# Performance work log

Measured on AMD Instinct MI355X. Metric: run time of the kernel, lower is better.

The kernel has to match this reference:

```python
import jax, jax.numpy as jnp
import numpy as np

B, T, C, H = 2, 2048, 1024, 16
D = C // H  # head_dim = 64


def setup_inputs() -> dict:
    key = jax.random.key(0)
    ks = jax.random.split(key, 5)
    s = 1.0 / np.sqrt(C)
    return {
        "x": jax.random.normal(ks[0], (B, T, C), jnp.float32),
        "Wq": jax.random.normal(ks[1], (C, C), jnp.float32) * s,
        "bq": jnp.zeros((C,), jnp.float32),
        "Wk": jax.random.normal(ks[2], (C, C), jnp.float32) * s,
        "bk": jnp.zeros((C,), jnp.float32),
        "Wv": jax.random.normal(ks[3], (C, C), jnp.float32) * s,
        "bv": jnp.zeros((C,), jnp.float32),
        "Wo": jax.random.normal(ks[4], (C, C), jnp.float32) * s,
        "bo": jnp.zeros((C,), jnp.float32),
    }


def reference(x, Wq, bq, Wk, bk, Wv, bv, Wo, bo):
    Bx, Tx, Cx = x.shape
    # torch Linear: y = x @ W.T + b
    q = (x @ Wq.T + bq).reshape(Bx, Tx, H, D).transpose(0, 2, 1, 3)  # [B,H,T,D]
    k = (x @ Wk.T + bk).reshape(Bx, Tx, H, D).transpose(0, 2, 1, 3)
    v = (x @ Wv.T + bv).reshape(Bx, Tx, H, D).transpose(0, 2, 1, 3)
    att = jnp.einsum("bhqd,bhkd->bhqk", q, k) / np.sqrt(D).astype(np.float32)
    mask = jnp.tril(jnp.ones((Tx, Tx), bool))  # causal mask [T,T]
    att = jnp.where(mask, att, -jnp.inf)
    att = jax.nn.softmax(att, axis=-1)
    out = jnp.einsum("bhqk,bhkd->bhqd", att, v)
    out = out.transpose(0, 2, 1, 3).reshape(Bx, Tx, Cx)
    return out @ Wo.T + bo
```

## Files before the change

### kernel.cpp

```cpp
#include <hip/hip_runtime.h>
#include <hip/hip_bf16.h>

#define B_ 2
#define T_ 2048
#define C_ 1024
#define H_ 16
#define D_ 64

typedef unsigned short u16;
typedef __bf16 bf16x8 __attribute__((ext_vector_type(8)));
typedef float floatx4 __attribute__((ext_vector_type(4)));

__device__ __forceinline__ float bf2f(u16 u) {
  union { unsigned int i; float f; } x; x.i = ((unsigned int)u) << 16; return x.f;
}
__device__ __forceinline__ u16 f2bf(float f) {
  union { float f; unsigned int i; } x; x.f = f;
  unsigned int r = x.i + 0x7fffu + ((x.i >> 16) & 1u);
  return (u16)(r >> 16);
}

__device__ __forceinline__ unsigned cvtpk(float lo, float hi) {
  unsigned r;
  asm("v_cvt_pk_bf16_f32 %0, %1, %2" : "=v"(r) : "v"(lo), "v"(hi));
  return r;
}

__device__ __forceinline__ void gld16(void* lds, const void* g) {
  __builtin_amdgcn_global_load_lds(
      (const __attribute__((address_space(1))) unsigned int*)g,
      (__attribute__((address_space(3))) unsigned int*)lds, 16, 0, 0);
}

#define NXF4 1048576
#define NWF4 262144

__global__ __launch_bounds__(256) void cvt_all(
    const float* __restrict__ x,  const float* __restrict__ Wq,
    const float* __restrict__ Wk, const float* __restrict__ Wv,
    const float* __restrict__ Wo, u16* __restrict__ dst_base)
{
  const int i = blockIdx.x * 256 + threadIdx.x;
  const float* src; size_t off;
  if (i < NXF4)               { src = x;  off = i; }
  else if (i < NXF4 + NWF4)   { src = Wq; off = i - NXF4; }
  else if (i < NXF4 + 2*NWF4) { src = Wk; off = i - (NXF4 + NWF4); }
  else if (i < NXF4 + 3*NWF4) { src = Wv; off = i - (NXF4 + 2*NWF4); }
  else                        { src = Wo; off = i - (NXF4 + 3*NWF4); }
  float4 f = ((const float4*)src)[off];
  ushort4 o;
  o.x = f2bf(f.x); o.y = f2bf(f.y); o.z = f2bf(f.z); o.w = f2bf(f.w);
  ((ushort4*)dst_base)[i] = o;
}

#define QSCALE 0.1803368801111f

#define PBAR()                                                \
  do {                                                        \
    asm volatile("" ::: "memory");                            \
    __builtin_amdgcn_s_barrier();                             \
    asm volatile("s_waitcnt lgkmcnt(0)" ::: "memory");        \
  } while (0)

#define EBAR()                                                \
  do {                                                        \
    asm volatile("" ::: "memory");                            \
    __builtin_amdgcn_s_barrier();                             \
    asm volatile("" ::: "memory");                            \
  } while (0)

__global__ __launch_bounds__(512, 2) void gemm_qkv8(
    const u16* __restrict__ X, const u16* __restrict__ Wb,
    const float* __restrict__ b0, const float* __restrict__ b1,
    const float* __restrict__ b2,
    u16* __restrict__ Yq, u16* __restrict__ Yk, u16* __restrict__ Yv)
{
  __shared__ __align__(16) u16 L[57344];

  const int tid  = threadIdx.x;
  const int lane = tid & 63;
  const int m16  = lane & 15;
  const int q4   = lane >> 4;
  const int wv   = tid >> 6;
  const int wm   = wv >> 2;
  const int wn   = wv & 3;

  const int bid = blockIdx.x;
  const int xcd = bid & 7;
  const int idx = bid >> 3;
  const int bx  = (xcd & 3) * 4 + (idx & 3);
  const int by  = (xcd >> 2) * 8 + (idx >> 2);

  const u16* Abase  = X  + (size_t)bx * 256 * C_;
  const u16* Bbase  = Wb + (size_t)by * 192 * C_;
  const u16* A1base = Abase + (size_t)128 * C_;

  const int rB  = tid >> 3;
  const int s0 = tid,       r0 = rB;
  const int s1 = tid + 512, r1 = 64 + rB;
  const int k0a = ((tid & 7) ^ (rB & 7)) * 8;

#define STAGE_A(dsthalf, srcrows, kofs)                                       \
  do {                                                                        \
    gld16(&(dsthalf)[s0 * 8], (srcrows) + (size_t)r0 * C_ + (kofs) + k0a);    \
    gld16(&(dsthalf)[s1 * 8], (srcrows) + (size_t)r1 * C_ + (kofs) + k0a);    \
  } while (0)

#define STAGE_BL(dstB, srcrows, kofs, l)                                      \
  gld16(&(dstB)[((l) * 512 + tid) * 8],                                       \
        (srcrows) + (size_t)((l) * 64 + rB) * C_ + (kofs) + k0a)

  u16* buf0 = L;
  u16* buf1 = L + 28672;

  STAGE_BL(buf0 + 16384, Bbase, 0, 0);
  STAGE_BL(buf0 + 16384, Bbase, 0, 1);
  STAGE_BL(buf0 + 16384, Bbase, 0, 2);
  STAGE_A (buf0,         Abase,  0);
  STAGE_A (buf0 + 8192,  A1base, 0);
  STAGE_BL(buf1 + 16384, Bbase, 64, 0);
  STAGE_BL(buf1 + 16384, Bbase, 64, 1);
  STAGE_A (buf1,         Abase, 64);
  asm volatile("s_waitcnt vmcnt(4)" ::: "memory");
  __builtin_amdgcn_s_barrier();
  asm volatile("" ::: "memory");

  floatx4 acc[8][3] = {};

  const int a0off = m16 * 64 + ((q4      ^ (lane & 7)) * 8);
  const int a1off = m16 * 64 + (((q4 + 4) ^ (lane & 7)) * 8);
  const int bro   = wn * 3072;

  for (int i = 0; i < 16; ++i) {
    u16* buf  = (i & 1) ? buf1 : buf0;
    u16* bufn = (i & 1) ? buf0 : buf1;
    const u16* Ah = buf + wm * 8192;
    const u16* Bh = buf + 16384;
    const bool p1 = (i + 1) < 16;
    const bool p2 = (i + 2) < 16;
    const int  k1 = (i + 1) * 64;
    const int  k2 = (i + 2) * 64;

    bf16x8 a[4][2], bA[2][2], bB[2];

#pragma unroll
    for (int f = 0; f < 4; ++f) {
      a[f][0] = *(const bf16x8*)&Ah[f * 1024 + a0off];
      a[f][1] = *(const bf16x8*)&Ah[f * 1024 + a1off];
    }
#pragma unroll
    for (int g = 0; g < 2; ++g) {
      bA[g][0] = *(const bf16x8*)&Bh[bro + g * 1024 + a0off];
      bA[g][1] = *(const bf16x8*)&Bh[bro + g * 1024 + a1off];
    }
    if (p1) STAGE_A(bufn + 8192, A1base, k1);
    PBAR();
    __builtin_amdgcn_s_setprio(1);
#pragma unroll
    for (int f = 0; f < 4; ++f)
#pragma unroll
      for (int g = 0; g < 2; ++g) {
        acc[f][g] = __builtin_amdgcn_mfma_f32_16x16x32_bf16(a[f][0], bA[g][0], acc[f][g], 0, 0, 0);
        acc[f][g] = __builtin_amdgcn_mfma_f32_16x16x32_bf16(a[f][1], bA[g][1], acc[f][g], 0, 0, 0);
      }
    __builtin_amdgcn_s_setprio(0);
    EBAR();

    bB[0] = *(const bf16x8*)&Bh[bro + 2048 + a0off];
    bB[1] = *(const bf16x8*)&Bh[bro + 2048 + a1off];
    if (p1) STAGE_BL(bufn + 16384, Bbase, k1, 2);
    PBAR();
    __builtin_amdgcn_s_setprio(1);
#pragma unroll
    for (int f = 0; f < 4; ++f) {
      acc[f][2] = __builtin_amdgcn_mfma_f32_16x16x32_bf16(a[f][0], bB[0], acc[f][2], 0, 0, 0);
      acc[f][2] = __builtin_amdgcn_mfma_f32_16x16x32_bf16(a[f][1], bB[1], acc[f][2], 0, 0, 0);
    }
    __builtin_amdgcn_s_setprio(0);
    EBAR();

#pragma unroll
    for (int f = 0; f < 4; ++f) {
      a[f][0] = *(const bf16x8*)&Ah[4096 + f * 1024 + a0off];
      a[f][1] = *(const bf16x8*)&Ah[4096 + f * 1024 + a1off];
    }
    if (p2) {
      STAGE_BL(buf + 16384, Bbase, k2, 0);
      STAGE_BL(buf + 16384, Bbase, k2, 1);
    }
    PBAR();
    __builtin_amdgcn_s_setprio(1);
#pragma unroll
    for (int f = 0; f < 4; ++f) {
      acc[4 + f][2] = __builtin_amdgcn_mfma_f32_16x16x32_bf16(a[f][0], bB[0], acc[4 + f][2], 0, 0, 0);
      acc[4 + f][2] = __builtin_amdgcn_mfma_f32_16x16x32_bf16(a[f][1], bB[1], acc[4 + f][2], 0, 0, 0);
    }
    __builtin_amdgcn_s_setprio(0);
    EBAR();

    if (p2) STAGE_A(buf, Abase, k2);
    PBAR();
    __builtin_amdgcn_s_setprio(1);
#pragma unroll
    for (int f = 0; f < 4; ++f)
#pragma unroll
      for (int g = 0; g < 2; ++g) {
        acc[4 + f][g] = __builtin_amdgcn_mfma_f32_16x16x32_bf16(a[f][0], bA[g][0], acc[4 + f][g], 0, 0, 0);
        acc[4 + f][g] = __builtin_amdgcn_mfma_f32_16x16x32_bf16(a[f][1], bA[g][1], acc[4 + f][g], 0, 0, 0);
      }
    __builtin_amdgcn_s_setprio(0);
    asm volatile("" ::: "memory");
    if (p2) asm volatile("s_waitcnt vmcnt(4)" ::: "memory");
    else    asm volatile("s_waitcnt vmcnt(0)" ::: "memory");
    __builtin_amdgcn_s_barrier();
    asm volatile("" ::: "memory");
  }

  const int mbase = bx * 256 + wm * 128 + q4 * 4;
#pragma unroll
  for (int nf = 0; nf < 3; ++nf) {
    const int nzg = by * 192 + wn * 48 + nf * 16 + m16;
    const int z  = nzg >> 10;
    const int nl = nzg & 1023;
    const int h = nl >> 6, d = nl & (D_ - 1);
    const float bv = (z == 0 ? b0 : z == 1 ? b1 : b2)[nl];
    if (z == 2) {
#pragma unroll
      for (int mf = 0; mf < 8; ++mf) {
        const int m  = mbase + mf * 16;
        const int bb = m >> 11, t = m & (T_ - 1);
        ushort4 pk;
        pk.x = f2bf(acc[mf][nf][0] + bv);
        pk.y = f2bf(acc[mf][nf][1] + bv);
        pk.z = f2bf(acc[mf][nf][2] + bv);
        pk.w = f2bf(acc[mf][nf][3] + bv);
        *(ushort4*)&Yv[(((size_t)bb * H_ + h) * D_ + d) * T_ + t] = pk;
      }
    } else {
      u16* Y = z ? Yk : Yq;
      const float sc = z ? 1.0f : QSCALE;
#pragma unroll
      for (int mf = 0; mf < 8; ++mf) {
        const int m  = mbase + mf * 16;
        const int bb = m >> 11, tq = m & (T_ - 1);
#pragma unroll
        for (int r = 0; r < 4; ++r) {
          Y[(((size_t)bb * H_ + h) * T_ + (tq + r)) * D_ + d] =
              f2bf((acc[mf][nf][r] + bv) * sc);
        }
      }
    }
  }
}

__global__ __launch_bounds__(256) void gemm_out(
    const u16* __restrict__ X, const u16* __restrict__ W,
    const float* __restrict__ bias, float* __restrict__ Yf)
{
  const int K = C_, N = C_;
  __shared__ __align__(16) u16 As[128 * 32];
  __shared__ __align__(16) u16 Bs[128 * 32];

  const int tid  = threadIdx.x;
  const int wv   = tid >> 6;
  const int lane = tid & 63;
  const int mcol = lane & 15;
  const int quad = lane >> 4;
  const int wr = wv >> 1, wc = wv & 1;
  const int m0 = blockIdx.x * 128;
  const int n0 = blockIdx.y * 128;

  const int srow = tid >> 2;
  const int scol = (tid & 3) * 8;
  const u16* xp0 = X + (size_t)(m0 + srow) * K + scol;
  const u16* xp1 = xp0 + (size_t)64 * K;
  const u16* wp0 = W + (size_t)(n0 + srow) * K + scol;
  const u16* wp1 = wp0 + (size_t)64 * K;

  floatx4 acc[4][4] = {};

  for (int k0 = 0; k0 < K; k0 += 32) {
    gld16(&As[tid * 8],        xp0 + k0);
    gld16(&As[2048 + tid * 8], xp1 + k0);
    gld16(&Bs[tid * 8],        wp0 + k0);
    gld16(&Bs[2048 + tid * 8], wp1 + k0);
    __syncthreads();

    bf16x8 a[4], b[4];
#pragma unroll
    for (int rf = 0; rf < 4; ++rf)
      a[rf] = *(const bf16x8*)&As[(wr * 64 + rf * 16 + mcol) * 32 + quad * 8];
#pragma unroll
    for (int cf = 0; cf < 4; ++cf)
      b[cf] = *(const bf16x8*)&Bs[(wc * 64 + cf * 16 + mcol) * 32 + quad * 8];
#pragma unroll
    for (int rf = 0; rf < 4; ++rf)
#pragma unroll
      for (int cf = 0; cf < 4; ++cf)
        acc[rf][cf] = __builtin_amdgcn_mfma_f32_16x16x32_bf16(
            a[rf], b[cf], acc[rf][cf], 0, 0, 0);
    __syncthreads();
  }

#pragma unroll
  for (int cf = 0; cf < 4; ++cf) {
    const int n = n0 + wc * 64 + cf * 16 + mcol;
    const float bv = bias[n];
#pragma unroll
    for (int rf = 0; rf < 4; ++rf) {
#pragma unroll
      for (int r = 0; r < 4; ++r) {
        const int m = m0 + wr * 64 + rf * 16 + quad * 4 + r;
        Yf[(size_t)m * N + n] = acc[rf][cf][r] + bv;
      }
    }
  }
}

#define KSB 4096
#define VTB 4096

__constant__ unsigned char CH_T[24]  = {7,15,15,14,14,6,13,13, 4,10,10,5,11,11,12,12, 9,9,8,8,3,2,1,0};
__constant__ unsigned char CH_J0[24] = {0,0,16,0,15,0,0,14,   0,0,11,0,0,12,0,13,    0,10,0,9,0,0,0,0};
__constant__ unsigned char CH_J1[24] = {15,15,31,14,29,13,13,27, 9,10,21,11,11,23,12,25, 9,19,8,17,7,5,3,1};
__constant__ unsigned char CH_P[24]  = {0,1,2,1,2,0,1,2,      0,1,2,0,1,2,1,2,       1,2,1,2,0,0,0,0};

__global__ __launch_bounds__(256, 3) void attn_flash(
    const u16* __restrict__ Q, const u16* __restrict__ K,
    const u16* __restrict__ Vg, u16* __restrict__ O,
    float* __restrict__ OP, float* __restrict__ LP)
{
  __shared__ __align__(16) u16 Ks[2 * KSB];
  __shared__ __align__(16) u16 Vt[2 * VTB];

  const int tid  = threadIdx.x;
  const int wv   = tid >> 6;
  const int lane = tid & 63;
  const int mcol = lane & 15;
  const int quad = lane >> 4;

  const int bx = blockIdx.x;
  const int bh = bx & 31;
  const int c  = bx >> 5;
  const int t  = CH_T[c];
  const int j0 = CH_J0[c];
  const int j1 = CH_J1[c];
  const int pm = CH_P[c];
  const int ti = pm ? ((bh * 8 + (t - 8)) * 2 + (pm - 1)) : 0;

  const size_t base  = (size_t)bh * T_ * D_;
  const size_t vbase = (size_t)bh * D_ * T_;
  const int b = bh >> 4, h = bh & (H_ - 1);

  bf16x8 vones;
  {
    const u16 ov = (mcol == 0) ? (u16)0x3F80 : (u16)0;
    union { u16 s[8]; bf16x8 v; } tmp;
#pragma unroll
    for (int i = 0; i < 8; ++i) tmp.s[i] = ov;
    vones = tmp.v;
  }

  const int srow = lane >> 3;
  const int sg   = (lane & 7) ^ srow;
  const int c0 = wv * 2, c1 = wv * 2 + 1;
  const int sl0 = (quad ^ (mcol & 7)) * 8;

  const size_t koff0 = base + (size_t)(c0 * 8 + srow) * D_ + sg * 8;
  const size_t koff1 = base + (size_t)(c1 * 8 + srow) * D_ + sg * 8;
  const size_t voff0 = vbase + (size_t)(c0 * 8 + srow) * T_ + sg * 8;
  const size_t voff1 = vbase + (size_t)(c1 * 8 + srow) * T_ + sg * 8;

  const u16* qg = Q + base + (size_t)(t * 128 + wv * 32 + mcol) * D_ + quad * 8;
  const bf16x8 qf[2][2] = {
    { *(const bf16x8*)qg,             *(const bf16x8*)(qg + 32) },
    { *(const bf16x8*)(qg + 16 * D_), *(const bf16x8*)(qg + 16 * D_ + 32) }
  };

  floatx4 oacc[2][5] = {};

  {
    const size_t kj = (size_t)j0 * 64 * D_;
    const int    vj = j0 * 64;
    gld16(&Ks[c0 * 512 + lane * 8], K  + koff0 + kj);
    gld16(&Ks[c1 * 512 + lane * 8], K  + koff1 + kj);
    gld16(&Vt[c0 * 512 + lane * 8], Vg + voff0 + vj);
    gld16(&Vt[c1 * 512 + lane * 8], Vg + voff1 + vj);
  }

  for (int j = j0; j <= j1; ++j) {
    const int cur = (j - j0) & 1;
    __syncthreads();

    if (j < j1) {
      const int nb = cur ^ 1;
      const size_t kj = (size_t)(j + 1) * 64 * D_;
      const int    vj = (j + 1) * 64;
      gld16(&Ks[nb * KSB + c0 * 512 + lane * 8], K  + koff0 + kj);
      gld16(&Ks[nb * KSB + c1 * 512 + lane * 8], K  + koff1 + kj);
      gld16(&Vt[nb * VTB + c0 * 512 + lane * 8], Vg + voff0 + vj);
      gld16(&Vt[nb * VTB + c1 * 512 + lane * 8], Vg + voff1 + vj);
    }

    const u16* ksb = &Ks[cur * KSB];
    const u16* vtb = &Vt[cur * VTB];

    floatx4 sacc[2][4] = {};
    __builtin_amdgcn_s_setprio(1);
#pragma unroll
    for (int nt = 0; nt < 4; ++nt) {
      const u16* kr = &ksb[(nt * 16 + mcol) * 64];
      bf16x8 kb0 = *(const bf16x8*)&kr[sl0];
      bf16x8 kb1 = *(const bf16x8*)&kr[sl0 ^ 32];
      sacc[0][nt] = __builtin_amdgcn_mfma_f32_16x16x32_bf16(kb0, qf[0][0], sacc[0][nt], 0, 0, 0);
      sacc[0][nt] = __builtin_amdgcn_mfma_f32_16x16x32_bf16(kb1, qf[0][1], sacc[0][nt], 0, 0, 0);
      sacc[1][nt] = __builtin_amdgcn_mfma_f32_16x16x32_bf16(kb0, qf[1][0], sacc[1][nt], 0, 0, 0);
      sacc[1][nt] = __builtin_amdgcn_mfma_f32_16x16x32_bf16(kb1, qf[1][1], sacc[1][nt], 0, 0, 0);
    }
    __builtin_amdgcn_s_setprio(0);

    const int dj = j - 2 * t;
    if (dj >= 0) {
#pragma unroll
      for (int hf = 0; hf < 2; ++hf) {
        const int klim = wv * 32 + hf * 16 + mcol - dj * 64;
#pragma unroll
        for (int nt = 0; nt < 4; ++nt)
#pragma unroll
          for (int r = 0; r < 4; ++r)
            if (nt * 16 + quad * 4 + r > klim) sacc[hf][nt][r] = -1e30f;
      }
    }

    bf16x8 pa[2][2];
#pragma unroll
    for (int hf = 0; hf < 2; ++hf) {
      unsigned w[4][2];
#pragma unroll
      for (int nt = 0; nt < 4; ++nt)
#pragma unroll
        for (int i = 0; i < 2; ++i)
          w[nt][i] = cvtpk(exp2f(sacc[hf][nt][2*i]), exp2f(sacc[hf][nt][2*i+1]));
      union { unsigned u[4]; bf16x8 v; } p0, p1;
#pragma unroll
      for (int i = 0; i < 2; ++i) {
        unsigned x = w[0][i], y = w[1][i];
        asm("v_permlane32_swap_b32 %0, %1" : "+v"(x), "+v"(y));
        asm("v_permlane16_swap_b32 %0, %1" : "+v"(x), "+v"(y));
        p0.u[i] = x; p0.u[i + 2] = y;
        unsigned x2 = w[2][i], y2 = w[3][i];
        asm("v_permlane32_swap_b32 %0, %1" : "+v"(x2), "+v"(y2));
        asm("v_permlane16_swap_b32 %0, %1" : "+v"(x2), "+v"(y2));
        p1.u[i] = x2; p1.u[i + 2] = y2;
      }
      pa[hf][0] = p0.v; pa[hf][1] = p1.v;
    }

    __builtin_amdgcn_s_setprio(1);
#pragma unroll
    for (int dt = 0; dt < 4; ++dt) {
      const u16* vr = &vtb[(dt * 16 + mcol) * 64];
      bf16x8 vb0 = *(const bf16x8*)&vr[sl0];
      bf16x8 vb1 = *(const bf16x8*)&vr[sl0 ^ 32];
      oacc[0][dt] = __builtin_amdgcn_mfma_f32_16x16x32_bf16(pa[0][0], vb0, oacc[0][dt], 0, 0, 0);
      oacc[0][dt] = __builtin_amdgcn_mfma_f32_16x16x32_bf16(pa[0][1], vb1, oacc[0][dt], 0, 0, 0);
      oacc[1][dt] = __builtin_amdgcn_mfma_f32_16x16x32_bf16(pa[1][0], vb0, oacc[1][dt], 0, 0, 0);
      oacc[1][dt] = __builtin_amdgcn_mfma_f32_16x16x32_bf16(pa[1][1], vb1, oacc[1][dt], 0, 0, 0);
    }
    oacc[0][4] = __builtin_amdgcn_mfma_f32_16x16x32_bf16(pa[0][0], vones, oacc[0][4], 0, 0, 0);
    oacc[0][4] = __builtin_amdgcn_mfma_f32_16x16x32_bf16(pa[0][1], vones, oacc[0][4], 0, 0, 0);
    oacc[1][4] = __builtin_amdgcn_mfma_f32_16x16x32_bf16(pa[1][0], vones, oacc[1][4], 0, 0, 0);
    oacc[1][4] = __builtin_amdgcn_mfma_f32_16x16x32_bf16(pa[1][1], vones, oacc[1][4], 0, 0, 0);
    __builtin_amdgcn_s_setprio(0);
  }

  if (!pm) {
#pragma unroll
    for (int hf = 0; hf < 2; ++hf) {
      float invl[4];
#pragma unroll
      for (int r = 0; r < 4; ++r)
        invl[r] = 1.f / __shfl(oacc[hf][4][r], lane & 48);
#pragma unroll
      for (int dt = 0; dt < 4; ++dt) {
        const int cc = h * D_ + dt * 16 + mcol;
#pragma unroll
        for (int r = 0; r < 4; ++r) {
          const int tg = t * 128 + wv * 32 + hf * 16 + quad * 4 + r;
          O[((size_t)b * T_ + tg) * C_ + cc] = f2bf(oacc[hf][dt][r] * invl[r]);
        }
      }
    }
  } else {
    float* op = OP + (size_t)ti * 8192;
#pragma unroll
    for (int hf = 0; hf < 2; ++hf) {
#pragma unroll
      for (int dt = 0; dt < 4; ++dt)
#pragma unroll
        for (int r = 0; r < 4; ++r)
          op[(wv * 32 + hf * 16 + quad * 4 + r) * 64 + dt * 16 + mcol] = oacc[hf][dt][r];
      if (mcol == 0) {
#pragma unroll
        for (int r = 0; r < 4; ++r)
          LP[ti * 128 + wv * 32 + hf * 16 + quad * 4 + r] = oacc[hf][4][r];
      }
    }
  }
}

__global__ __launch_bounds__(256) void attn_merge(
    const float* __restrict__ OP, const float* __restrict__ LP,
    u16* __restrict__ O)
{
  const int mb = blockIdx.x;
  const int bh = mb & 31, tt = mb >> 5;
  const int t = 8 + tt;
  const int ti0 = (bh * 8 + tt) * 2;
  const int b = bh >> 4, h = bh & (H_ - 1);
  const int row = threadIdx.x >> 1;
  const int dc  = (threadIdx.x & 1) * 32;

  const float l = LP[ti0 * 128 + row] + LP[(ti0 + 1) * 128 + row];
  const float inv = 1.f / l;
  const float* pa = OP + (size_t)ti0 * 8192 + row * 64 + dc;
  const float* pb = pa + 8192;

  const int tg = t * 128 + row;
  u16* o = O + ((size_t)b * T_ + tg) * C_ + h * D_ + dc;

  u16 tmp[32];
#pragma unroll
  for (int i = 0; i < 8; ++i) {
    const float4 a4 = ((const float4*)pa)[i];
    const float4 b4 = ((const float4*)pb)[i];
    tmp[i*4 + 0] = f2bf((a4.x + b4.x) * inv);
    tmp[i*4 + 1] = f2bf((a4.y + b4.y) * inv);
    tmp[i*4 + 2] = f2bf((a4.z + b4.z) * inv);
    tmp[i*4 + 3] = f2bf((a4.w + b4.w) * inv);
  }
#pragma unroll
  for (int i = 0; i < 4; ++i)
    ((uint4*)o)[i] = ((const uint4*)tmp)[i];
}

extern "C" void kernel_launch(void* const* d_in, const int* in_sizes, int n_in,
                              void* d_out, int out_size, void* d_ws, size_t ws_size,
                              hipStream_t stream) {
  const float* x  = (const float*)d_in[0];
  const float* Wq = (const float*)d_in[1];
  const float* bq = (const float*)d_in[2];
  const float* Wk = (const float*)d_in[3];
  const float* bk = (const float*)d_in[4];
  const float* Wv = (const float*)d_in[5];
  const float* bv = (const float*)d_in[6];
  const float* Wo = (const float*)d_in[7];
  const float* bo = (const float*)d_in[8];
  float* out = (float*)d_out;

  const size_t NX = (size_t)B_ * T_ * C_;
  const size_t NW = (size_t)C_ * C_;

  u16* xb  = (u16*)d_ws;
  u16* wqb = xb  + NX;
  u16* wkb = wqb + NW;
  u16* wvb = wkb + NW;
  u16* wob = wvb + NW;
  u16* q   = wob + NW;
  u16* k   = q   + NX;
  u16* v   = k   + NX;
  u16* ctx = v   + NX;
  float* opart = (float*)(ctx + NX);
  float* lpart = opart + (size_t)512 * 8192;

  cvt_all<<<dim3((NXF4 + 4 * NWF4) / 256), 256, 0, stream>>>(x, Wq, Wk, Wv, Wo, xb);

  gemm_qkv8<<<dim3(256), 512, 0, stream>>>(xb, wqb, bq, bk, bv, q, k, v);

  attn_flash<<<dim3(768), 256, 0, stream>>>(q, k, v, ctx, opart, lpart);

  attn_merge<<<dim3(256), 256, 0, stream>>>(opart, lpart, ctx);

  gemm_out<<<dim3(32, 8), 256, 0, stream>>>(ctx, wob, bo, out);
}
```

Measured before the change: 185.4 us.

## Triple-buffer K/V tiles in flash attention with explicit vmcnt waits

```diff
diff --git a/kernel.cpp b/kernel.cpp
--- a/kernel.cpp
+++ b/kernel.cpp
@@ -330,8 +330,8 @@
     const u16* __restrict__ Vg, u16* __restrict__ O,
     float* __restrict__ OP, float* __restrict__ LP)
 {
-  __shared__ __align__(16) u16 Ks[2 * KSB];
-  __shared__ __align__(16) u16 Vt[2 * VTB];
+  __shared__ __align__(16) u16 Ks[3 * KSB];
+  __shared__ __align__(16) u16 Vt[3 * VTB];
 
   const int tid  = threadIdx.x;
   const int wv   = tid >> 6;
@@ -379,27 +379,30 @@
 
   floatx4 oacc[2][5] = {};
 
-  {
-    const size_t kj = (size_t)j0 * 64 * D_;
-    const int    vj = j0 * 64;
-    gld16(&Ks[c0 * 512 + lane * 8], K  + koff0 + kj);
-    gld16(&Ks[c1 * 512 + lane * 8], K  + koff1 + kj);
-    gld16(&Vt[c0 * 512 + lane * 8], Vg + voff0 + vj);
-    gld16(&Vt[c1 * 512 + lane * 8], Vg + voff1 + vj);
-  }
-
+#define STG_KV(bufi, jt)                                                      \
+  do {                                                                        \
+    const size_t kj_ = (size_t)(jt) * 64 * D_;                                \
+    const int    vj_ = (jt) * 64;                                             \
+    gld16(&Ks[(bufi) * KSB + c0 * 512 + lane * 8], K  + koff0 + kj_);         \
+    gld16(&Ks[(bufi) * KSB + c1 * 512 + lane * 8], K  + koff1 + kj_);         \
+    gld16(&Vt[(bufi) * VTB + c0 * 512 + lane * 8], Vg + voff0 + vj_);         \
+    gld16(&Vt[(bufi) * VTB + c1 * 512 + lane * 8], Vg + voff1 + vj_);         \
+  } while (0)
+
+  STG_KV(0, j0);
+  if (j0 + 1 <= j1) STG_KV(1, j0 + 1);
+
+  int cur = 0;
   for (int j = j0; j <= j1; ++j) {
-    const int cur = (j - j0) & 1;
-    __syncthreads();
-
-    if (j < j1) {
-      const int nb = cur ^ 1;
-      const size_t kj = (size_t)(j + 1) * 64 * D_;
-      const int    vj = (j + 1) * 64;
-      gld16(&Ks[nb * KSB + c0 * 512 + lane * 8], K  + koff0 + kj);
-      gld16(&Ks[nb * KSB + c1 * 512 + lane * 8], K  + koff1 + kj);
-      gld16(&Vt[nb * VTB + c0 * 512 + lane * 8], Vg + voff0 + vj);
-      gld16(&Vt[nb * VTB + c1 * 512 + lane * 8], Vg + voff1 + vj);
+    asm volatile("" ::: "memory");
+    if (j < j1) asm volatile("s_waitcnt vmcnt(4)" ::: "memory");
+    else        asm volatile("s_waitcnt vmcnt(0)" ::: "memory");
+    __builtin_amdgcn_s_barrier();
+    asm volatile("" ::: "memory");
+
+    if (j + 2 <= j1) {
+      int nb = cur + 2; if (nb >= 3) nb -= 3;
+      STG_KV(nb, j + 2);
     }
 
     const u16* ksb = &Ks[cur * KSB];
@@ -472,6 +475,8 @@
     oacc[1][4] = __builtin_amdgcn_mfma_f32_16x16x32_bf16(pa[1][0], vones, oacc[1][4], 0, 0, 0);
     oacc[1][4] = __builtin_amdgcn_mfma_f32_16x16x32_bf16(pa[1][1], vones, oacc[1][4], 0, 0, 0);
     __builtin_amdgcn_s_setprio(0);
+
+    cur = (cur == 2) ? 0 : cur + 1;
   }
 
   if (!pm) {
```

New measurement: 184.7 us. Within noise of the previous version (-0.3%).
